# Performance work log

Hardware: AMD Instinct MI355X
Metric: run time of the kernel (lower is better)

The kernel has to match this reference:

```python
import jax, jax.numpy as jnp
import numpy as np

B = 16384          # batch (positions)
F = 32             # active features per perspective per sample
INPUT_SIZE = 40960
HIDDEN_SIZE = 256
L2_SIZE = 32


def _embedding_bag_sum(weight, indices, offsets, num_bags):
    """torch.nn.EmbeddingBag(mode='sum') with offsets."""
    n = indices.shape[0]
    # segment id of each flat index: which bag it belongs to
    seg = jnp.searchsorted(offsets, jnp.arange(n), side='right') - 1
    return jax.ops.segment_sum(weight[indices], seg, num_segments=num_bags)


def setup_inputs() -> dict:
    key = jax.random.key(0)
    ks = jax.random.split(key, 6)
    white_indices = jax.random.randint(ks[0], (B * F,), 0, INPUT_SIZE)
    black_indices = jax.random.randint(ks[1], (B * F,), 0, INPUT_SIZE)
    offsets = jnp.arange(B, dtype=jnp.int64 if jax.config.jax_enable_x64 else jnp.int32) * F
    stm = jax.random.bernoulli(ks[2], 0.5, (B,))
    ft_weight = jax.random.uniform(ks[3], (INPUT_SIZE, HIDDEN_SIZE), minval=-0.05, maxval=0.05)
    ft_bias = jnp.zeros((HIDDEN_SIZE,), jnp.float32)
    # kaiming_normal (fan_in mode) approximations
    l1_w = jax.random.normal(ks[4], (L2_SIZE, 2 * HIDDEN_SIZE)) * np.float32(np.sqrt(2.0 / (2 * HIDDEN_SIZE)))
    l1_b = jnp.zeros((L2_SIZE,), jnp.float32)
    l2_w = jax.random.normal(ks[5], (1, L2_SIZE)) * np.float32(np.sqrt(1.0 / L2_SIZE))
    l2_b = jnp.zeros((1,), jnp.float32)
    return {
        'white_indices': white_indices, 'white_offsets': offsets,
        'black_indices': black_indices, 'black_offsets': offsets,
        'stm': stm,
        'ft_weight': ft_weight, 'ft_bias': ft_bias,
        'l1_w': l1_w, 'l1_b': l1_b, 'l2_w': l2_w, 'l2_b': l2_b,
    }


def reference(white_indices, white_offsets, black_indices, black_offsets, stm,
              ft_weight, ft_bias, l1_w, l1_b, l2_w, l2_b):
    nb = white_offsets.shape[0]
    white_acc = _embedding_bag_sum(ft_weight, white_indices, white_offsets, nb) + ft_bias
    black_acc = _embedding_bag_sum(ft_weight, black_indices, black_offsets, nb) + ft_bias
    white_acc = jnp.clip(white_acc, 0.0, 1.0)
    black_acc = jnp.clip(black_acc, 0.0, 1.0)
    stm_col = stm[:, None]
    us = jnp.where(stm_col, black_acc, white_acc)
    them = jnp.where(stm_col, white_acc, black_acc)
    combined = jnp.concatenate([us, them], axis=1)          # [B, 2H]
    hidden = jnp.clip(combined @ l1_w.T + l1_b, 0.0, 1.0)   # [B, L2]
    return hidden @ l2_w.T + l2_b                            # [B, 1]
```

## Files before the change

kernel.cpp:

```cpp
#include <hip/hip_runtime.h>
#include <hip/hip_fp16.h>


typedef _Float16 h2 __attribute__((ext_vector_type(2)));
typedef float    fx4 __attribute__((ext_vector_type(4)));
typedef unsigned ux4 __attribute__((ext_vector_type(4)));

#define QSCALE 2048.0f
#define QINV   (1.0f / 2048.0f)
#define TBL_BYTES  (40960ull * 256ull)
#define FEAT_BYTES (16384ull * 512ull * 2ull)

__device__ __forceinline__ float clamp01(float x) { return fminf(fmaxf(x, 0.0f), 1.0f); }

__device__ __forceinline__ float fdot2f(h2 a, h2 b, float c) {
#if __has_builtin(__builtin_amdgcn_fdot2)
    return __builtin_amdgcn_fdot2(a, b, c, false);
#else
    return c + (float)a.x * (float)b.x + (float)a.y * (float)b.y;
#endif
}
__device__ __forceinline__ unsigned pk2(float lo, float hi) {
    h2 v; v.x = (_Float16)lo; v.y = (_Float16)hi;
    return __builtin_bit_cast(unsigned, v);
}
__device__ __forceinline__ h2 as_h2(unsigned u) { return __builtin_bit_cast(h2, u); }
__device__ __forceinline__ unsigned short f16b(float x) {
    return __builtin_bit_cast(unsigned short, (_Float16)x);
}

__device__ __forceinline__ void acc4(unsigned d, int& a0, int& a1, int& a2, int& a3) {
#if __has_builtin(__builtin_amdgcn_sdot4)
    a0 = __builtin_amdgcn_sdot4((int)d, 0x00000001, a0, false);
    a1 = __builtin_amdgcn_sdot4((int)d, 0x00000100, a1, false);
    a2 = __builtin_amdgcn_sdot4((int)d, 0x00010000, a2, false);
    a3 = __builtin_amdgcn_sdot4((int)d, 0x01000000, a3, false);
#else
    a0 += (int)(signed char)(d);
    a1 += (int)(signed char)(d >> 8);
    a2 += (int)(signed char)(d >> 16);
    a3 += (int)(signed char)(d >> 24);
#endif
}

__device__ __forceinline__ unsigned pkb(fx4 v) {
    const int q0 = __float2int_rn(v.x * QSCALE) & 255;
    const int q1 = __float2int_rn(v.y * QSCALE) & 255;
    const int q2 = __float2int_rn(v.z * QSCALE) & 255;
    const int q3 = __float2int_rn(v.w * QSCALE) & 255;
    return (unsigned)(q0 | (q1 << 8) | (q2 << 16) | (q3 << 24));
}
__global__ __launch_bounds__(256)
void cvt_f32_i8(const fx4* __restrict__ src, ux4* __restrict__ dst, int n16) {
    const int i = blockIdx.x * 256 + threadIdx.x;
    if (i >= n16) return;
    const fx4 a = __builtin_nontemporal_load(&src[4 * i]);
    const fx4 b = __builtin_nontemporal_load(&src[4 * i + 1]);
    const fx4 c = __builtin_nontemporal_load(&src[4 * i + 2]);
    const fx4 d = __builtin_nontemporal_load(&src[4 * i + 3]);
    ux4 o; o.x = pkb(a); o.y = pkb(b); o.z = pkb(c); o.w = pkb(d);
    __builtin_nontemporal_store(o, &dst[i]);
}

#define FOLDA(T, arr, NK, M)                                         \
    _Pragma("unroll")                                                \
    for (int k_ = 0; k_ < (NK) / 2; ++k_) {                          \
        const T fa_ = arr[k_], fb_ = arr[k_ + (NK) / 2];             \
        const T send_ = (lane & (M)) ? fa_ : fb_;                    \
        const T recv_ = __shfl_xor(send_, (M), 64);                  \
        arr[k_] = ((lane & (M)) ? fb_ : fa_) + recv_;                \
    }

__global__ __launch_bounds__(256, 8)
void nnue_gather(const int* __restrict__ wi, const int* __restrict__ bi,
                 const void* __restrict__ stmv,
                 const ux4* __restrict__ t4,
                 const float* __restrict__ ftbf,
                 unsigned short* __restrict__ feat)
{
    const int tid  = threadIdx.x;
    const int lane = tid & 63;
    const int g     = blockIdx.x;
    const int chunk = g & 3;
    const int half  = (g >> 2) & 1;
    const int grp   = g >> 3;

    const unsigned sprobe = __builtin_nontemporal_load(&((const unsigned*)stmv)[lane]);
    const unsigned long long isf32 = __ballot(sprobe == 0x3f800000u);
    const unsigned long long isbig = __ballot(sprobe > 1u);
    const int smode = isf32 ? 2 : (isbig ? 1 : 0);

    const int c_l = ((lane & 3) << 4) | (((lane >> 2) & 1) << 3)
                  | (((lane >> 3) & 1) << 2) | (((lane >> 4) & 1) << 1)
                  | (lane >> 5);
    const int colg = chunk * 64 + c_l;
    const float bias = ftbf[colg];

    const int lq = lane >> 2;
    const int lh = lane & 3;
    const int tb = chunk * 4 + lh;

    const int b0base = half * 8192 + grp * 32 + (tid >> 6) * 8;
    const int* __restrict__ ip = (lane < 32) ? wi : bi;

    int vidx = __builtin_nontemporal_load(&ip[(b0base << 5) + (lane & 31)]);

    for (int bb = 0; bb < 8; ++bb) {
        const int b = b0base + bb;
        int vnext = 0;
        if (bb < 7)
            vnext = __builtin_nontemporal_load(&ip[((b + 1) << 5) + (lane & 31)]);

        const int iw0 = __shfl(vidx, lq, 64);
        const int iw1 = __shfl(vidx, 16 + lq, 64);
        const int ib0 = __shfl(vidx, 32 + lq, 64);
        const int ib1 = __shfl(vidx, 48 + lq, 64);
        const ux4 rw0 = t4[iw0 * 16 + tb];
        const ux4 rw1 = t4[iw1 * 16 + tb];
        const ux4 rb0 = t4[ib0 * 16 + tb];
        const ux4 rb1 = t4[ib1 * 16 + tb];

        int wv[16], bv[16];
#pragma unroll
        for (int i = 0; i < 16; ++i) { wv[i] = 0; bv[i] = 0; }
        acc4(rw0.x, wv[0], wv[1], wv[2], wv[3]);
        acc4(rw0.y, wv[4], wv[5], wv[6], wv[7]);
        acc4(rw0.z, wv[8], wv[9], wv[10], wv[11]);
        acc4(rw0.w, wv[12], wv[13], wv[14], wv[15]);
        acc4(rw1.x, wv[0], wv[1], wv[2], wv[3]);
        acc4(rw1.y, wv[4], wv[5], wv[6], wv[7]);
        acc4(rw1.z, wv[8], wv[9], wv[10], wv[11]);
        acc4(rw1.w, wv[12], wv[13], wv[14], wv[15]);
        acc4(rb0.x, bv[0], bv[1], bv[2], bv[3]);
        acc4(rb0.y, bv[4], bv[5], bv[6], bv[7]);
        acc4(rb0.z, bv[8], bv[9], bv[10], bv[11]);
        acc4(rb0.w, bv[12], bv[13], bv[14], bv[15]);
        acc4(rb1.x, bv[0], bv[1], bv[2], bv[3]);
        acc4(rb1.y, bv[4], bv[5], bv[6], bv[7]);
        acc4(rb1.z, bv[8], bv[9], bv[10], bv[11]);
        acc4(rb1.w, bv[12], bv[13], bv[14], bv[15]);

        FOLDA(int, wv, 16, 4)  FOLDA(int, bv, 16, 4)
        FOLDA(int, wv, 8, 8)   FOLDA(int, bv, 8, 8)
        FOLDA(int, wv, 4, 16)  FOLDA(int, bv, 4, 16)
        FOLDA(int, wv, 2, 32)  FOLDA(int, bv, 2, 32)

        const float W  = clamp01((float)wv[0] * QINV + bias);
        const float Bk = clamp01((float)bv[0] * QINV + bias);

        int s;
        if (smode == 0)      s = __builtin_nontemporal_load(&((const int*)stmv)[b]);
        else if (smode == 1) s = __builtin_nontemporal_load(&((const unsigned char*)stmv)[b]);
        else                 s = (__builtin_nontemporal_load(&((const float*)stmv)[b]) != 0.0f);

        const float us = s ? Bk : W;
        const float th = s ? W : Bk;
        __builtin_nontemporal_store(f16b(us), &feat[b * 512 + colg]);
        __builtin_nontemporal_store(f16b(th), &feat[b * 512 + 256 + colg]);

        vidx = vnext;
    }
}

__global__ __launch_bounds__(256, 4)
void nnue_mlp(const ux4* __restrict__ feat4,
              const float4* __restrict__ l1w,
              const float* __restrict__ l1b,
              const float* __restrict__ l2w,
              const float* __restrict__ l2b,
              float* __restrict__ out)
{
    __shared__ uint2 pkA[64 * 32];
    __shared__ uint2 pkB[64 * 32];
    __shared__ float lbS[32];
    __shared__ float lwS[32];
    __shared__ float l2bS;

    const int tid  = threadIdx.x;
    const int lane = tid & 63;
    const int lm   = lane & 31;

    {
        const int kg = tid >> 6;
#pragma unroll
        for (int i = 0; i < 8; ++i) {
            const int k = kg * 8 + i;
            const float4 a = l1w[k * 128 + 2 * lane];
            const float4 c = l1w[k * 128 + 2 * lane + 1];
            const int sw = lane * 32 + (k ^ lm);
            pkA[sw] = make_uint2(pk2(a.x, a.y), pk2(a.z, a.w));
            pkB[sw] = make_uint2(pk2(c.x, c.y), pk2(c.z, c.w));
        }
        if (tid < 32) { lbS[tid] = l1b[tid]; lwS[tid] = l2w[tid]; }
        if (tid == 0) l2bS = l2b[0];
    }
    __syncthreads();

    const int b = blockIdx.x * 4 + (tid >> 6);

    const ux4 f = __builtin_nontemporal_load(&feat4[b * 64 + lane]);
    const h2 f0 = as_h2(f.x), f1 = as_h2(f.y), f2 = as_h2(f.z), f3 = as_h2(f.w);

    const uint2* __restrict__ pa = pkA + lane * 32;
    const uint2* __restrict__ pb = pkB + lane * 32;

    float hid[32];
#pragma unroll
    for (int k = 0; k < 32; ++k) {
        const uint2 wa = pa[k ^ lm];
        const uint2 wb = pb[k ^ lm];
        float s = fdot2f(as_h2(wa.x), f0, 0.0f);
        s = fdot2f(as_h2(wa.y), f1, s);
        s = fdot2f(as_h2(wb.x), f2, s);
        hid[k] = fdot2f(as_h2(wb.y), f3, s);
    }

    FOLDA(float, hid, 32, 32)
    FOLDA(float, hid, 16, 16)
    FOLDA(float, hid, 8, 8)
    FOLDA(float, hid, 4, 4)
    FOLDA(float, hid, 2, 2)
    const float S = hid[0] + __shfl_xor(hid[0], 1, 64);
    const int kk = (lane >> 1) & 31;

    float v = clamp01(S + lbS[kk]) * lwS[kk];
#pragma unroll
    for (int m = 2; m <= 32; m <<= 1) v += __shfl_xor(v, m, 64);

    if (lane == 0) out[b] = v + l2bS;
}

template <int TBL>
__global__ __launch_bounds__(256, 4)
void nnue_fused(const int* __restrict__ wi, const int* __restrict__ bi,
                const void* __restrict__ stmv, const void* __restrict__ tblv,
                const float4* __restrict__ ftb, const float4* __restrict__ l1w,
                const float* __restrict__ l1b, const float* __restrict__ l2w,
                const float* __restrict__ l2b, float* __restrict__ out)
{
    __shared__ uint2 pk_us[64 * 32];
    __shared__ uint2 pk_th[64 * 32];
    __shared__ float lbS[32];
    __shared__ float lwS[32];
    __shared__ float l2bS;

    const int tid  = threadIdx.x;
    const int lane = tid & 63;
    const int lm   = lane & 31;
    {
        const int kg = tid >> 6;
#pragma unroll
        for (int i = 0; i < 8; ++i) {
            const int k  = kg * 8 + i;
            const float4 u = l1w[k * 128 + lane];
            const float4 t = l1w[k * 128 + 64 + lane];
            const int sw = lane * 32 + (k ^ lm);
            pk_us[sw] = make_uint2(pk2(u.x, u.y), pk2(u.z, u.w));
            pk_th[sw] = make_uint2(pk2(t.x, t.y), pk2(t.z, t.w));
        }
        if (tid < 32) { lbS[tid] = l1b[tid]; lwS[tid] = l2w[tid]; }
        if (tid == 0) l2bS = l2b[0];
    }
    __syncthreads();

    const unsigned sprobe = ((const unsigned*)stmv)[lane];
    const unsigned long long isf32 = __ballot(sprobe == 0x3f800000u);
    const unsigned long long isbig = __ballot(sprobe > 1u);
    const int smode = isf32 ? 2 : (isbig ? 1 : 0);

    const int gw = blockIdx.x * 4 + (tid >> 6);
    const int q  = lane >> 2;
    const int r  = lane & 3;
    const float4 bvv = ftb[lane];
    const uint2* __restrict__ pu = pk_us + lane * 32;
    const uint2* __restrict__ pt = pk_th + lane * 32;

    for (int bb = 0; bb < 4; ++bb) {
        const int b = gw * 4 + bb;
        const int vidx = ((lane < 32) ? wi : bi)[(b << 5) + lm];
        float aw0, aw1, aw2, aw3, ab0, ab1, ab2, ab3;

        if (TBL == 1) {
            const uint4* __restrict__ t4 = (const uint4*)tblv;
            int iw[8], ib[8];
#pragma unroll
            for (int jj = 0; jj < 8; ++jj) {
                iw[jj] = __shfl(vidx, 4 * jj + r, 64);
                ib[jj] = __shfl(vidx, 32 + 4 * jj + r, 64);
            }
            int wa[16], ba[16];
#pragma unroll
            for (int i = 0; i < 16; ++i) { wa[i] = 0; ba[i] = 0; }
#pragma unroll
            for (int jj = 0; jj < 8; ++jj) {
                const uint4 rw = t4[iw[jj] * 16 + q];
                acc4(rw.x, wa[0], wa[1], wa[2], wa[3]);
                acc4(rw.y, wa[4], wa[5], wa[6], wa[7]);
                acc4(rw.z, wa[8], wa[9], wa[10], wa[11]);
                acc4(rw.w, wa[12], wa[13], wa[14], wa[15]);
            }
#pragma unroll
            for (int jj = 0; jj < 8; ++jj) {
                const uint4 rb = t4[ib[jj] * 16 + q];
                acc4(rb.x, ba[0], ba[1], ba[2], ba[3]);
                acc4(rb.y, ba[4], ba[5], ba[6], ba[7]);
                acc4(rb.z, ba[8], ba[9], ba[10], ba[11]);
                acc4(rb.w, ba[12], ba[13], ba[14], ba[15]);
            }
#pragma unroll
            for (int i = 0; i < 16; ++i) {
                wa[i] += __shfl_xor(wa[i], 1, 64);
                ba[i] += __shfl_xor(ba[i], 1, 64);
            }
#pragma unroll
            for (int i = 0; i < 16; ++i) {
                wa[i] += __shfl_xor(wa[i], 2, 64);
                ba[i] += __shfl_xor(ba[i], 2, 64);
            }
            int ws_[4], bs[4];
#pragma unroll
            for (int j = 0; j < 4; ++j) {
                const int wlo = (lane & 1) ? wa[4 + j]  : wa[j];
                const int whi = (lane & 1) ? wa[12 + j] : wa[8 + j];
                ws_[j] = (lane & 2) ? whi : wlo;
                const int blo = (lane & 1) ? ba[4 + j]  : ba[j];
                const int bhi = (lane & 1) ? ba[12 + j] : ba[8 + j];
                bs[j] = (lane & 2) ? bhi : blo;
            }
            aw0 = (float)ws_[0] * QINV; aw1 = (float)ws_[1] * QINV;
            aw2 = (float)ws_[2] * QINV; aw3 = (float)ws_[3] * QINV;
            ab0 = (float)bs[0] * QINV;  ab1 = (float)bs[1] * QINV;
            ab2 = (float)bs[2] * QINV;  ab3 = (float)bs[3] * QINV;
        } else {
            const float4* __restrict__ tbl = (const float4*)tblv;
            aw0 = aw1 = aw2 = aw3 = 0.f;
            ab0 = ab1 = ab2 = ab3 = 0.f;
#pragma unroll 8
            for (int j = 0; j < 32; ++j) {
                const int iw  = __builtin_amdgcn_readlane(vidx, j);
                const int ibk = __builtin_amdgcn_readlane(vidx, j + 32);
                const float4 rw = tbl[iw * 64 + lane];
                const float4 rb = tbl[ibk * 64 + lane];
                aw0 += rw.x; aw1 += rw.y; aw2 += rw.z; aw3 += rw.w;
                ab0 += rb.x; ab1 += rb.y; ab2 += rb.z; ab3 += rb.w;
            }
        }

        aw0 = clamp01(aw0 + bvv.x); aw1 = clamp01(aw1 + bvv.y);
        aw2 = clamp01(aw2 + bvv.z); aw3 = clamp01(aw3 + bvv.w);
        ab0 = clamp01(ab0 + bvv.x); ab1 = clamp01(ab1 + bvv.y);
        ab2 = clamp01(ab2 + bvv.z); ab3 = clamp01(ab3 + bvv.w);

        int s;
        if (smode == 0)      s = ((const int*)stmv)[b];
        else if (smode == 1) s = ((const unsigned char*)stmv)[b];
        else                 s = (((const float*)stmv)[b] != 0.0f);

        const float u0 = s ? ab0 : aw0, u1 = s ? ab1 : aw1;
        const float u2 = s ? ab2 : aw2, u3 = s ? ab3 : aw3;
        const float t0 = s ? aw0 : ab0, t1 = s ? aw1 : ab1;
        const float t2 = s ? aw2 : ab2, t3 = s ? aw3 : ab3;

        h2 u01; u01.x = (_Float16)u0; u01.y = (_Float16)u1;
        h2 u23; u23.x = (_Float16)u2; u23.y = (_Float16)u3;
        h2 t01; t01.x = (_Float16)t0; t01.y = (_Float16)t1;
        h2 t23; t23.x = (_Float16)t2; t23.y = (_Float16)t3;

        float hid[32];
#pragma unroll
        for (int k = 0; k < 32; ++k) {
            const uint2 wu = pu[k ^ lm];
            const uint2 wt = pt[k ^ lm];
            float sacc = fdot2f(as_h2(wu.x), u01, 0.0f);
            sacc = fdot2f(as_h2(wu.y), u23, sacc);
            sacc = fdot2f(as_h2(wt.x), t01, sacc);
            hid[k] = fdot2f(as_h2(wt.y), t23, sacc);
        }

        FOLDA(float, hid, 32, 32)
        FOLDA(float, hid, 16, 16)
        FOLDA(float, hid, 8, 8)
        FOLDA(float, hid, 4, 4)
        FOLDA(float, hid, 2, 2)
        const float S = hid[0] + __shfl_xor(hid[0], 1, 64);
        const int kk = (lane >> 1) & 31;

        float v = clamp01(S + lbS[kk]) * lwS[kk];
#pragma unroll
        for (int m = 2; m <= 32; m <<= 1) v += __shfl_xor(v, m, 64);

        if (lane == 0) out[b] = v + l2bS;
    }
}

extern "C" void kernel_launch(void* const* d_in, const int* in_sizes, int n_in,
                              void* d_out, int out_size, void* d_ws, size_t ws_size,
                              hipStream_t stream) {
    const int*    wi  = (const int*)d_in[0];
    const int*    bi  = (const int*)d_in[2];
    const void*   stm = d_in[4];
    const float*  ftw = (const float*)d_in[5];
    const float*  ftbf = (const float*)d_in[6];
    const float4* l1w = (const float4*)d_in[7];
    const float*  l1b = (const float*)d_in[8];
    const float*  l2w = (const float*)d_in[9];
    const float*  l2b = (const float*)d_in[10];
    float* out = (float*)d_out;

    const int n16 = (40960 * 256) / 16;

    if (ws_size >= TBL_BYTES + FEAT_BYTES) {
        unsigned short* feat = (unsigned short*)((char*)d_ws + TBL_BYTES);
        hipLaunchKernelGGL(cvt_f32_i8, dim3(n16 / 256), dim3(256), 0, stream,
                           (const fx4*)ftw, (ux4*)d_ws, n16);
        hipLaunchKernelGGL(nnue_gather, dim3(2048), dim3(256), 0, stream,
                           wi, bi, stm, (const ux4*)d_ws, ftbf, feat);
        hipLaunchKernelGGL(nnue_mlp, dim3(4096), dim3(256), 0, stream,
                           (const ux4*)feat, l1w, l1b, l2w, l2b, out);
    } else if (ws_size >= TBL_BYTES) {
        hipLaunchKernelGGL(cvt_f32_i8, dim3(n16 / 256), dim3(256), 0, stream,
                           (const fx4*)ftw, (ux4*)d_ws, n16);
        hipLaunchKernelGGL((nnue_fused<1>), dim3(1024), dim3(256), 0, stream,
                           wi, bi, stm, (const void*)d_ws, (const float4*)ftbf,
                           l1w, l1b, l2w, l2b, out);
    } else {
        hipLaunchKernelGGL((nnue_fused<0>), dim3(1024), dim3(256), 0, stream,
                           wi, bi, stm, (const void*)ftw, (const float4*)ftbf,
                           l1w, l1b, l2w, l2b, out);
    }
}
```

Before: 174.6 us.

## Split int8 table into per-chunk column slabs and use cached stores for intermediates

The int8 quantized feature table is rewritten as four contiguous column-chunk slabs, so each gather block reads rows from a compact 40960x64-byte region instead of striding through the full 256-byte row. This shrinks the per-block working set and is meant to improve L2/MALL hit rates for the random row gathers. The feature buffer stores in the gather kernel and its loads in the MLP kernel switch from nontemporal to normal cached accesses, so the intermediate can stay in cache between kernels. The table conversion stores also lose their nontemporal hint.

```diff
diff --git a/kernel.cpp b/kernel.cpp
--- a/kernel.cpp
+++ b/kernel.cpp
@@ -10,6 +10,7 @@
 #define QINV   (1.0f / 2048.0f)
 #define TBL_BYTES  (40960ull * 256ull)
 #define FEAT_BYTES (16384ull * 512ull * 2ull)
+#define CHUNK_UX4  (40960 * 4)
 
 __device__ __forceinline__ float clamp01(float x) { return fminf(fmaxf(x, 0.0f), 1.0f); }
 
@@ -50,6 +51,7 @@
     const int q3 = __float2int_rn(v.w * QSCALE) & 255;
     return (unsigned)(q0 | (q1 << 8) | (q2 << 16) | (q3 << 24));
 }
+template <int SPLIT>
 __global__ __launch_bounds__(256)
 void cvt_f32_i8(const fx4* __restrict__ src, ux4* __restrict__ dst, int n16) {
     const int i = blockIdx.x * 256 + threadIdx.x;
@@ -59,7 +61,14 @@
     const fx4 c = __builtin_nontemporal_load(&src[4 * i + 2]);
     const fx4 d = __builtin_nontemporal_load(&src[4 * i + 3]);
     ux4 o; o.x = pkb(a); o.y = pkb(b); o.z = pkb(c); o.w = pkb(d);
-    __builtin_nontemporal_store(o, &dst[i]);
+    if (SPLIT) {
+        const int row   = i >> 4;
+        const int sub   = i & 3;
+        const int chunk = (i >> 2) & 3;
+        dst[chunk * CHUNK_UX4 + row * 4 + sub] = o;
+    } else {
+        dst[i] = o;
+    }
 }
 
 #define FOLDA(T, arr, NK, M)                                         \
@@ -74,7 +83,7 @@
 __global__ __launch_bounds__(256, 8)
 void nnue_gather(const int* __restrict__ wi, const int* __restrict__ bi,
                  const void* __restrict__ stmv,
-                 const ux4* __restrict__ t4,
+                 const ux4* __restrict__ tbl,
                  const float* __restrict__ ftbf,
                  unsigned short* __restrict__ feat)
 {
@@ -98,7 +107,7 @@
 
     const int lq = lane >> 2;
     const int lh = lane & 3;
-    const int tb = chunk * 4 + lh;
+    const ux4* __restrict__ tc = tbl + chunk * CHUNK_UX4;
 
     const int b0base = half * 8192 + grp * 32 + (tid >> 6) * 8;
     const int* __restrict__ ip = (lane < 32) ? wi : bi;
@@ -115,10 +124,10 @@
         const int iw1 = __shfl(vidx, 16 + lq, 64);
         const int ib0 = __shfl(vidx, 32 + lq, 64);
         const int ib1 = __shfl(vidx, 48 + lq, 64);
-        const ux4 rw0 = t4[iw0 * 16 + tb];
-        const ux4 rw1 = t4[iw1 * 16 + tb];
-        const ux4 rb0 = t4[ib0 * 16 + tb];
-        const ux4 rb1 = t4[ib1 * 16 + tb];
+        const ux4 rw0 = tc[iw0 * 4 + lh];
+        const ux4 rw1 = tc[iw1 * 4 + lh];
+        const ux4 rb0 = tc[ib0 * 4 + lh];
+        const ux4 rb1 = tc[ib1 * 4 + lh];
 
         int wv[16], bv[16];
 #pragma unroll
@@ -155,8 +164,8 @@
 
         const float us = s ? Bk : W;
         const float th = s ? W : Bk;
-        __builtin_nontemporal_store(f16b(us), &feat[b * 512 + colg]);
-        __builtin_nontemporal_store(f16b(th), &feat[b * 512 + 256 + colg]);
+        feat[b * 512 + colg]       = f16b(us);
+        feat[b * 512 + 256 + colg] = f16b(th);
 
         vidx = vnext;
     }
@@ -198,7 +207,7 @@
 
     const int b = blockIdx.x * 4 + (tid >> 6);
 
-    const ux4 f = __builtin_nontemporal_load(&feat4[b * 64 + lane]);
+    const ux4 f = feat4[b * 64 + lane];
     const h2 f0 = as_h2(f.x), f1 = as_h2(f.y), f2 = as_h2(f.z), f3 = as_h2(f.w);
 
     const uint2* __restrict__ pa = pkA + lane * 32;
@@ -411,14 +420,14 @@
 
     if (ws_size >= TBL_BYTES + FEAT_BYTES) {
         unsigned short* feat = (unsigned short*)((char*)d_ws + TBL_BYTES);
-        hipLaunchKernelGGL(cvt_f32_i8, dim3(n16 / 256), dim3(256), 0, stream,
+        hipLaunchKernelGGL((cvt_f32_i8<1>), dim3(n16 / 256), dim3(256), 0, stream,
                            (const fx4*)ftw, (ux4*)d_ws, n16);
         hipLaunchKernelGGL(nnue_gather, dim3(2048), dim3(256), 0, stream,
                            wi, bi, stm, (const ux4*)d_ws, ftbf, feat);
         hipLaunchKernelGGL(nnue_mlp, dim3(4096), dim3(256), 0, stream,
                            (const ux4*)feat, l1w, l1b, l2w, l2b, out);
     } else if (ws_size >= TBL_BYTES) {
-        hipLaunchKernelGGL(cvt_f32_i8, dim3(n16 / 256), dim3(256), 0, stream,
+        hipLaunchKernelGGL((cvt_f32_i8<0>), dim3(n16 / 256), dim3(256), 0, stream,
                            (const fx4*)ftw, (ux4*)d_ws, n16);
         hipLaunchKernelGGL((nnue_fused<1>), dim3(1024), dim3(256), 0, stream,
                            wi, bi, stm, (const void*)d_ws, (const float4*)ftbf,
```

New measurement: 168.4 us. 3.5% less time.
